# Kernel tuning notes

Measured on AMD Instinct MI355X. Metric: run time of the kernel, lower is better.

## Reference

```python
import jax, jax.numpy as jnp
import numpy as np
import math

B, S, E, H, L, VOCAB, OUT = 32, 1024, 512, 8, 2, 20000, 1
D = E // H


def positional_encoding(seq_length, embed_size):
    position = jnp.arange(seq_length, dtype=jnp.float32)[:, None]
    div_term = jnp.exp(jnp.arange(0, embed_size, 2, dtype=jnp.float32) * (-math.log(10000.0) / embed_size))
    pe = jnp.zeros((seq_length, embed_size), dtype=jnp.float32)
    pe = pe.at[:, 0::2].set(jnp.sin(position * div_term))
    pe = pe.at[:, 1::2].set(jnp.cos(position * div_term))
    return pe


def setup_inputs() -> dict:
    key = jax.random.key(0)
    ks = jax.random.split(key, 12)
    inputs = jax.random.randint(ks[0], (B, S), 0, VOCAB)
    s = 1.0 / math.sqrt(E)
    embed_table = jax.random.normal(ks[1], (VOCAB, E), jnp.float32)
    embed_table = embed_table.at[0].set(0.0)  # padding_idx=0
    # per-layer Q,K,V,O linear weights [L,E,E] (applied as x @ W + b) and biases [L,E]
    Wq = jax.random.normal(ks[2], (L, E, E), jnp.float32) * s
    Wk = jax.random.normal(ks[3], (L, E, E), jnp.float32) * s
    Wv = jax.random.normal(ks[4], (L, E, E), jnp.float32) * s
    Wo = jax.random.normal(ks[5], (L, E, E), jnp.float32) * s
    bq = jax.random.normal(ks[6], (L, E), jnp.float32) * s
    bk = jax.random.normal(ks[7], (L, E), jnp.float32) * s
    bv = jax.random.normal(ks[8], (L, E), jnp.float32) * s
    bo = jax.random.normal(ks[9], (L, E), jnp.float32) * s
    W_out = jax.random.normal(ks[10], (E, OUT), jnp.float32) * s
    b_out = jax.random.normal(ks[11], (OUT,), jnp.float32) * s
    return {"inputs": inputs, "embed_table": embed_table, "Wq": Wq, "bq": bq,
            "Wk": Wk, "bk": bk, "Wv": Wv, "bv": bv, "Wo": Wo, "bo": bo,
            "W_out": W_out, "b_out": b_out}


def _mha(x, Wq, bq, Wk, bk, Wv, bv, Wo, bo, mask):
    b, s = x.shape[:2]
    def heads(W, bias):
        return (x @ W + bias).reshape(b, s, H, D).transpose(0, 2, 1, 3)  # [b,H,s,D]
    q, k, v = heads(Wq, bq), heads(Wk, bk), heads(Wv, bv)
    scores = jnp.einsum('bhqd,bhkd->bhqk', q, k) / math.sqrt(D)
    scores = jnp.where(mask, -1e9, scores)
    prob = jax.nn.softmax(scores, axis=-1)
    out = jnp.einsum('bhqk,bhkd->bhqd', prob, v)
    out = out.transpose(0, 2, 1, 3).reshape(b, s, E)
    return out @ Wo + bo


def reference(inputs, embed_table, Wq, bq, Wk, bk, Wv, bv, Wo, bo, W_out, b_out):
    embeds = embed_table[inputs]  # [B,S,E]
    embeds = embeds + positional_encoding(inputs.shape[1], embeds.shape[-1])
    mask = jnp.triu(jnp.ones((inputs.shape[1], inputs.shape[1]), bool), k=1)  # future mask
    out = embeds
    for l in range(L):
        attn = _mha(out, Wq[l], bq[l], Wk[l], bk[l], Wv[l], bv[l], Wo[l], bo[l], mask)
        out = out + jax.nn.relu(attn)  # dropout is identity (eval / p=0)
    return out @ W_out + b_out
```

## Files before the change

kernel.cpp:

```cpp
#include <hip/hip_runtime.h>

typedef unsigned short u16;
typedef unsigned int u32;
using short8  = __attribute__((ext_vector_type(8))) short;
using floatx4 = __attribute__((ext_vector_type(4))) float;

#define NB 32
#define SEQ 1024
#define EMB 512
#define NH 8
#define HD 64
#define NLAYER 2
#define M_ROWS (NB * SEQ)

__device__ __forceinline__ float bf2f(u16 u) {
  union { u32 i; float f; } v; v.i = ((u32)u) << 16; return v.f;
}
__device__ __forceinline__ u16 f2bf(float f) {
  union { float f; u32 i; } v; v.f = f;
  u32 r = v.i + 0x7fffu + ((v.i >> 16) & 1u);
  return (u16)(r >> 16);
}

#if __has_builtin(__builtin_amdgcn_exp2f)
#define EXP2F __builtin_amdgcn_exp2f
#else
#define EXP2F exp2f
#endif

typedef __attribute__((address_space(3))) unsigned int lds_u32_t;
typedef __attribute__((address_space(1))) const unsigned int gbl_u32_t;
__device__ __forceinline__ void gload16(void* lds, const void* g) {
  gbl_u32_t* gp = (gbl_u32_t*)(unsigned long long)g;
  lds_u32_t* lp = (lds_u32_t*)(unsigned int)(unsigned long long)lds;
  __builtin_amdgcn_global_load_lds(gp, lp, 16, 0, 0);
}

__global__ void prep_weights(const float* __restrict__ Wq, const float* __restrict__ Wk,
                             const float* __restrict__ Wv, const float* __restrict__ Wo,
                             u16* __restrict__ WtQKV, u16* __restrict__ WtO) {
  int idx = blockIdx.x * 256 + threadIdx.x;
  const int QKV_TOT = NLAYER * 3 * EMB * EMB;
  if (idx < QKV_TOT) {
    int l = idx / (3 * EMB * EMB);
    int rem = idx % (3 * EMB * EMB);
    int n = rem / EMB, kk = rem % EMB;
    int w = n >> 9, e = n & 511;
    const float* src = (w == 0) ? Wq : (w == 1) ? Wk : Wv;
    WtQKV[idx] = f2bf(src[((size_t)l * EMB + kk) * EMB + e]);
  } else {
    int j = idx - QKV_TOT;
    int l = j / (EMB * EMB);
    int rem = j % (EMB * EMB);
    int n = rem / EMB, kk = rem % EMB;
    WtO[j] = f2bf(Wo[((size_t)l * EMB + kk) * EMB + n]);
  }
}

__global__ void embed_pe(const int* __restrict__ inp, const float* __restrict__ table,
                         u16* __restrict__ x) {
  int row = blockIdx.x;
  int tok = inp[row];
  int s = row & (SEQ - 1);
  const float negln = -9.210340371976184f / (float)EMB;
  for (int e = threadIdx.x; e < EMB; e += blockDim.x) {
    float val = table[(size_t)tok * EMB + e];
    int i = e >> 1;
    float dt = __expf((float)(2 * i) * negln);
    float ang = (float)s * dt;
    float pe = (e & 1) ? __cosf(ang) : __sinf(ang);
    x[(size_t)row * EMB + e] = f2bf(val + pe);
  }
}

#define BK 32

__global__ __launch_bounds__(256) void gemm_bt(
    const u16* __restrict__ A, const u16* __restrict__ Bt, int K, int mode,
    const float* bias0, const float* bias1, const float* bias2,
    u16* out0, u16* out1, u16* out2, const u16* resid, int Nstride) {
  __shared__ u16 sA[2][128][BK];
  __shared__ u16 sB[2][128][BK];
  int tid = threadIdx.x;
  int wave = tid >> 6, lane = tid & 63;
  int quad = lane >> 4, l16 = lane & 15;
  int wm = wave >> 1, wn = wave & 1;

  int NT = (mode == 0) ? 12 : 4;
  int blk = blockIdx.x;
  int xcd = blk & 7, slot = blk >> 3;
  int mtl = slot / NT, ntl = slot % NT;
  int bm0 = (xcd * 32 + mtl) * 128;
  int bn0 = ntl * 128;
  bool vswap = (mode == 0) && (bn0 >= 1024);

  floatx4 acc[4][4];
#pragma unroll
  for (int i = 0; i < 4; ++i)
#pragma unroll
    for (int j = 0; j < 4; ++j) acc[i][j] = (floatx4){0.f, 0.f, 0.f, 0.f};

  int rb = wave * 32;
  int lrow = lane >> 2;
  int gcg = ((lane & 3) ^ ((lane >> 3) & 3)) * 8;
  int rsl = (quad ^ ((l16 >> 1) & 3)) * 8;

  const u16* Arow0 = &A[(size_t)(bm0 + rb + lrow) * K + gcg];
  const u16* Arow1 = &A[(size_t)(bm0 + rb + 16 + lrow) * K + gcg];
  const u16* Brow0 = &Bt[(size_t)(bn0 + rb + lrow) * K + gcg];
  const u16* Brow1 = &Bt[(size_t)(bn0 + rb + 16 + lrow) * K + gcg];

  gload16(&sA[0][rb][0],      Arow0);
  gload16(&sA[0][rb + 16][0], Arow1);
  gload16(&sB[0][rb][0],      Brow0);
  gload16(&sB[0][rb + 16][0], Brow1);

  const int niter = K / BK;
  int ibuf = 0;
  for (int it = 0; it < niter; ++it) {
    if (it + 1 < niter) {
      int k1 = (it + 1) * BK;
      int nb = ibuf ^ 1;
      gload16(&sA[nb][rb][0],      Arow0 + k1);
      gload16(&sA[nb][rb + 16][0], Arow1 + k1);
      gload16(&sB[nb][rb][0],      Brow0 + k1);
      gload16(&sB[nb][rb + 16][0], Brow1 + k1);
      asm volatile("s_waitcnt vmcnt(4)" ::: "memory");
    } else {
      asm volatile("s_waitcnt vmcnt(0)" ::: "memory");
    }
    asm volatile("s_barrier" ::: "memory");

    short8 af[4], bfr[4];
#pragma unroll
    for (int mi = 0; mi < 4; ++mi)
      af[mi] = *(const short8*)&sA[ibuf][wm * 64 + mi * 16 + l16][rsl];
#pragma unroll
    for (int ni = 0; ni < 4; ++ni)
      bfr[ni] = *(const short8*)&sB[ibuf][wn * 64 + ni * 16 + l16][rsl];
    if (!vswap) {
#pragma unroll
      for (int mi = 0; mi < 4; ++mi)
#pragma unroll
        for (int ni = 0; ni < 4; ++ni)
          acc[mi][ni] = __builtin_amdgcn_mfma_f32_16x16x32_bf16(af[mi], bfr[ni], acc[mi][ni], 0, 0, 0);
    } else {
#pragma unroll
      for (int mi = 0; mi < 4; ++mi)
#pragma unroll
        for (int ni = 0; ni < 4; ++ni)
          acc[mi][ni] = __builtin_amdgcn_mfma_f32_16x16x32_bf16(bfr[ni], af[mi], acc[mi][ni], 0, 0, 0);
    }
    asm volatile("s_waitcnt lgkmcnt(0)" ::: "memory");
    asm volatile("s_barrier" ::: "memory");
    ibuf ^= 1;
  }

  u16* scr = ((u16*)sA) + wave * (16 * 68);
  int erow = lane >> 5;
  int dcol = lane & 31;

  if (!vswap) {
    int w = bn0 >> 9;
    const float* bp = (mode == 1) ? bias0 : ((w == 0) ? bias0 : bias1);
    float sc = (mode == 0 && w == 0) ? 0.18033688011112042f : 1.0f;
    float bv[4];
#pragma unroll
    for (int ni = 0; ni < 4; ++ni)
      bv[ni] = bp[(bn0 + wn * 64 + ni * 16 + l16) & 511];

#pragma unroll
    for (int mi = 0; mi < 4; ++mi) {
#pragma unroll
      for (int ni = 0; ni < 4; ++ni)
#pragma unroll
        for (int r = 0; r < 4; ++r) {
          float t = (acc[mi][ni][r] + bv[ni]) * sc;
          if (mode == 1) t = fmaxf(t, 0.f);
          scr[(quad * 4 + r) * 68 + ni * 16 + l16] = f2bf(t);
        }
      asm volatile("s_waitcnt lgkmcnt(0)" ::: "memory");

      int m0 = bm0 + wm * 64 + mi * 16;
      int colg = bn0 + wn * 64 + dcol * 2;
#pragma unroll
      for (int p = 0; p < 8; ++p) {
        int row = p * 2 + erow;
        u32 d2 = *(const u32*)&scr[row * 68 + dcol * 2];
        int m = m0 + row;
        if (mode == 0) {
          int e = colg & 511, h = e >> 6, d = e & 63;
          int b = m >> 10, sid = m & 1023;
          u16* optr = (w == 0) ? out0 : out1;
          *(u32*)&optr[((size_t)(b * NH + h) * SEQ + sid) * HD + d] = d2;
        } else {
          size_t off = (size_t)m * Nstride + colg;
          u32 rs = *(const u32*)&resid[off];
          float lo = bf2f((u16)d2) + bf2f((u16)rs);
          float hi = bf2f((u16)(d2 >> 16)) + bf2f((u16)(rs >> 16));
          *(u32*)&out0[off] = ((u32)f2bf(hi) << 16) | f2bf(lo);
        }
      }
      asm volatile("s_waitcnt lgkmcnt(0)" ::: "memory");
    }
  } else {
    float bvv[4][4];
#pragma unroll
    for (int ni = 0; ni < 4; ++ni)
#pragma unroll
      for (int r = 0; r < 4; ++r)
        bvv[ni][r] = bias2[(bn0 + wn * 64 + ni * 16 + quad * 4 + r) & 511];

    int b = (bm0 + wm * 64) >> 10;
    int sid0 = (bm0 + wm * 64) & 1023;
    int n0 = bn0 + wn * 64;
    int h = (n0 >> 6) & 7;
#pragma unroll
    for (int ni = 0; ni < 4; ++ni) {
#pragma unroll
      for (int mi = 0; mi < 4; ++mi)
#pragma unroll
        for (int r = 0; r < 4; ++r)
          scr[(quad * 4 + r) * 68 + mi * 16 + l16] = f2bf(acc[mi][ni][r] + bvv[ni][r]);
      asm volatile("s_waitcnt lgkmcnt(0)" ::: "memory");

      int d0 = (n0 & 63) + ni * 16;
#pragma unroll
      for (int p = 0; p < 8; ++p) {
        int row = p * 2 + erow;
        u32 d2 = *(const u32*)&scr[row * 68 + dcol * 2];
        *(u32*)&out2[((size_t)(b * NH + h) * HD + d0 + row) * SEQ + sid0 + dcol * 2] = d2;
      }
      asm volatile("s_waitcnt lgkmcnt(0)" ::: "memory");
    }
  }
}

#define RD8(T, row, cg) (*(const short8*)&(T)[(size_t)(row) * 64 + ((((cg) ^ ((row) & 7))) * 8)])

__global__ __launch_bounds__(256) void attn_kernel(
    const u16* __restrict__ q, const u16* __restrict__ k, const u16* __restrict__ vt,
    u16* __restrict__ o) {
  int blk = blockIdx.x;
  int xcd = blk & 7, slot = blk >> 3;
  int bh = xcd * 32 + (slot >> 3);
  int qtp = 7 - (slot & 7);
  int b = bh >> 3, h = bh & 7;
  int qA0 = qtp * 128, qB0 = qA0 + 64;

  __shared__ u16 smem[25088];
  u16* sQ = smem;
  u16* sK = smem;
  u16* sV = smem + 8192;
  u16* sP = smem + 16384;

  int tid = threadIdx.x, wave = tid >> 6, lane = tid & 63;
  int quad = lane >> 4, l16 = lane & 15;
  int rr = lane >> 3, gc8 = ((lane & 7) ^ rr) * 8;

  const u16* qbase = &q[((size_t)bh * SEQ + qA0) * HD];
  const u16* kbase = &k[(size_t)bh * SEQ * HD];
  const u16* vbase = &vt[(size_t)bh * HD * SEQ];

#pragma unroll
  for (int c = 0; c < 2; ++c) {
    int row0 = wave * 16 + c * 8;
    gload16(sQ + row0 * 64,        qbase + (size_t)(row0 + rr) * HD + gc8);
    gload16(sQ + (64 + row0) * 64, qbase + (size_t)(64 + row0 + rr) * HD + gc8);
  }
  asm volatile("s_waitcnt vmcnt(0)" ::: "memory");
  asm volatile("s_barrier" ::: "memory");
  short8 aqA0, aqA1, aqB0, aqB1;
  {
    int ra = wave * 16 + l16;
    aqA0 = RD8(sQ, ra, quad);
    aqA1 = RD8(sQ, ra, 4 + quad);
    aqB0 = RD8(sQ + 4096, ra, quad);
    aqB1 = RD8(sQ + 4096, ra, 4 + quad);
  }
  asm volatile("s_waitcnt lgkmcnt(0)" ::: "memory");
  asm volatile("s_barrier" ::: "memory");

  const u16* kp0 = kbase + (size_t)(wave * 16 + rr) * HD + gc8;
  const u16* kp1 = kp0 + 8 * HD;
  const u16* vp0 = vbase + (size_t)(wave * 16 + rr) * SEQ + gc8;
  const u16* vp1 = vp0 + 8 * SEQ;

  short8 ones;
#pragma unroll
  for (int j = 0; j < 8; ++j) ones[j] = (short)0x3F80;

  floatx4 accoA[4], accoB[4], accsumA, accsumB;
#pragma unroll
  for (int i = 0; i < 4; ++i) {
    accoA[i] = (floatx4){0.f, 0.f, 0.f, 0.f};
    accoB[i] = (floatx4){0.f, 0.f, 0.f, 0.f};
  }
  accsumA = (floatx4){0.f, 0.f, 0.f, 0.f};
  accsumB = (floatx4){0.f, 0.f, 0.f, 0.f};

  auto process = [&](short8 aq0, short8 aq1, int qX0, bool diag, int sub,
                     floatx4* acco, floatx4& accsum, int k0,
                     const u16* Kc, const u16* Vc) {
    floatx4 accs[4];
#pragma unroll
    for (int i = 0; i < 4; ++i) accs[i] = (floatx4){0.f, 0.f, 0.f, 0.f};
#pragma unroll
    for (int nt = 0; nt < 4; ++nt) {
      int rbk = nt * 16 + l16;
      accs[nt] = __builtin_amdgcn_mfma_f32_16x16x32_bf16(aq0, RD8(Kc, rbk, quad), accs[nt], 0, 0, 0);
      accs[nt] = __builtin_amdgcn_mfma_f32_16x16x32_bf16(aq1, RD8(Kc, rbk, 4 + quad), accs[nt], 0, 0, 0);
    }
    int prowbase = sub * 4352 + (wave * 16 + quad * 4) * 68;
    if (!diag) {
#pragma unroll
      for (int nt = 0; nt < 4; ++nt)
#pragma unroll
        for (int r = 0; r < 4; ++r) {
          float p = EXP2F(fminf(accs[nt][r], 108.f));
          sP[prowbase + r * 68 + nt * 16 + l16] = (u16)(__float_as_uint(p) >> 16);
        }
    } else {
      int qg_base = qX0 + wave * 16 + quad * 4;
#pragma unroll
      for (int nt = 0; nt < 4; ++nt) {
        int kg = k0 + nt * 16 + l16;
#pragma unroll
        for (int r = 0; r < 4; ++r) {
          float p = EXP2F(fminf(accs[nt][r], 108.f));
          if (kg > qg_base + r) p = 0.f;
          sP[prowbase + r * 68 + nt * 16 + l16] = (u16)(__float_as_uint(p) >> 16);
        }
      }
    }
    asm volatile("s_waitcnt lgkmcnt(0)" ::: "memory");
#pragma unroll
    for (int cst = 0; cst < 2; ++cst) {
      short8 ap = *(const short8*)&sP[sub * 4352 + (wave * 16 + l16) * 68 + cst * 32 + quad * 8];
#pragma unroll
      for (int dt = 0; dt < 4; ++dt) {
        int rv = dt * 16 + l16;
        acco[dt] = __builtin_amdgcn_mfma_f32_16x16x32_bf16(ap, RD8(Vc, rv, cst * 4 + quad), acco[dt], 0, 0, 0);
      }
      accsum = __builtin_amdgcn_mfma_f32_16x16x32_bf16(ap, ones, accsum, 0, 0, 0);
    }
  };

  {
    int row0 = wave * 16;
    gload16(sK + row0 * 64,       kp0);
    gload16(sK + (row0 + 8) * 64, kp1);
    gload16(sV + row0 * 64,       vp0);
    gload16(sV + (row0 + 8) * 64, vp1);
  }

  int ktmax = 2 * qtp + 1;
  int cur = 0;
  for (int kt = 0; kt <= ktmax; ++kt) {
    if (kt < ktmax) {
      int nb = cur ^ 1;
      size_t ko = (size_t)(kt + 1) * (64 * HD);
      size_t vo = (size_t)(kt + 1) * 64;
      int row0 = wave * 16;
      gload16(sK + nb * 4096 + row0 * 64,       kp0 + ko);
      gload16(sK + nb * 4096 + (row0 + 8) * 64, kp1 + ko);
      gload16(sV + nb * 4096 + row0 * 64,       vp0 + vo);
      gload16(sV + nb * 4096 + (row0 + 8) * 64, vp1 + vo);
      asm volatile("s_waitcnt vmcnt(4)" ::: "memory");
    } else {
      asm volatile("s_waitcnt vmcnt(0)" ::: "memory");
    }
    asm volatile("s_barrier" ::: "memory");

    const u16* Kc = sK + cur * 4096;
    const u16* Vc = sV + cur * 4096;
    int k0 = kt * 64;
    if (kt <= 2 * qtp)
      process(aqA0, aqA1, qA0, kt == 2 * qtp, 0, accoA, accsumA, k0, Kc, Vc);
    process(aqB0, aqB1, qB0, kt == ktmax, 1, accoB, accsumB, k0, Kc, Vc);

    asm volatile("s_waitcnt lgkmcnt(0)" ::: "memory");
    asm volatile("s_barrier" ::: "memory");
    cur ^= 1;
  }

#pragma unroll
  for (int dt = 0; dt < 4; ++dt)
#pragma unroll
    for (int r = 0; r < 4; ++r) {
      int rowoff = wave * 16 + quad * 4 + r;
      int col = h * HD + dt * 16 + l16;
      o[((size_t)b * SEQ + qA0 + rowoff) * EMB + col] = f2bf(accoA[dt][r] / accsumA[r]);
      o[((size_t)b * SEQ + qB0 + rowoff) * EMB + col] = f2bf(accoB[dt][r] / accsumB[r]);
    }
}

__global__ __launch_bounds__(256) void out_proj(const u16* __restrict__ x,
                                                const float* __restrict__ wout,
                                                const float* __restrict__ bout,
                                                float* __restrict__ out) {
  int wave = threadIdx.x >> 6, lane = threadIdx.x & 63;
  int m = blockIdx.x * 4 + wave;
  union { uint4 vv; u16 s[8]; } xv;
  xv.vv = *(const uint4*)&x[(size_t)m * EMB + lane * 8];
  float4 w0 = *(const float4*)&wout[lane * 8];
  float4 w1 = *(const float4*)&wout[lane * 8 + 4];
  float wv[8] = {w0.x, w0.y, w0.z, w0.w, w1.x, w1.y, w1.z, w1.w};
  float s = 0.f;
#pragma unroll
  for (int j = 0; j < 8; ++j) s += bf2f(xv.s[j]) * wv[j];
#pragma unroll
  for (int sh = 1; sh < 64; sh <<= 1) s += __shfl_xor(s, sh, 64);
  if (lane == 0) out[m] = s + bout[0];
}

extern "C" void kernel_launch(void* const* d_in, const int* in_sizes, int n_in,
                              void* d_out, int out_size, void* d_ws, size_t ws_size,
                              hipStream_t stream) {
  const int*   inp   = (const int*)d_in[0];
  const float* table = (const float*)d_in[1];
  const float* Wq    = (const float*)d_in[2];
  const float* bq    = (const float*)d_in[3];
  const float* Wk    = (const float*)d_in[4];
  const float* bk    = (const float*)d_in[5];
  const float* Wv    = (const float*)d_in[6];
  const float* bv    = (const float*)d_in[7];
  const float* Wo    = (const float*)d_in[8];
  const float* bo    = (const float*)d_in[9];
  const float* Wout  = (const float*)d_in[10];
  const float* bout  = (const float*)d_in[11];
  float* outp = (float*)d_out;

  char* ws = (char*)d_ws;
  const size_t SZ = (size_t)M_ROWS * EMB * 2;
  u16* x      = (u16*)(ws);
  u16* qb     = (u16*)(ws + SZ);
  u16* kb     = (u16*)(ws + 2 * SZ);
  u16* vb     = (u16*)(ws + 3 * SZ);
  u16* attn_b = (u16*)(ws + 4 * SZ);
  u16* WtQKV  = (u16*)(ws + 5 * SZ);
  u16* WtO    = (u16*)(ws + 5 * SZ + (size_t)NLAYER * 3 * EMB * EMB * 2);

  prep_weights<<<8192, 256, 0, stream>>>(Wq, Wk, Wv, Wo, WtQKV, WtO);
  embed_pe<<<M_ROWS, 256, 0, stream>>>(inp, table, x);

  for (int l = 0; l < NLAYER; ++l) {
    gemm_bt<<<3072, 256, 0, stream>>>(
        x, WtQKV + (size_t)l * 3 * EMB * EMB, EMB, 0,
        bq + l * EMB, bk + l * EMB, bv + l * EMB, qb, kb, vb, nullptr, 0);
    attn_kernel<<<2048, 256, 0, stream>>>(qb, kb, vb, attn_b);
    gemm_bt<<<1024, 256, 0, stream>>>(
        attn_b, WtO + (size_t)l * EMB * EMB, EMB, 1,
        bo + l * EMB, nullptr, nullptr, x, nullptr, nullptr, x, EMB);
  }
  out_proj<<<8192, 256, 0, stream>>>(x, Wout, bout, outp);
}
```

Measured before the change: 688.7 us.

## Drop K/V double buffering and share P buffer to halve attention LDS

```diff
diff --git a/kernel.cpp b/kernel.cpp
--- a/kernel.cpp
+++ b/kernel.cpp
@@ -248,11 +248,11 @@
   int b = bh >> 3, h = bh & 7;
   int qA0 = qtp * 128, qB0 = qA0 + 64;
 
-  __shared__ u16 smem[25088];
+  __shared__ u16 smem[12544];
   u16* sQ = smem;
   u16* sK = smem;
-  u16* sV = smem + 8192;
-  u16* sP = smem + 16384;
+  u16* sV = smem + 4096;
+  u16* sP = smem + 8192;
 
   int tid = threadIdx.x, wave = tid >> 6, lane = tid & 63;
   int quad = lane >> 4, l16 = lane & 15;
@@ -268,8 +268,7 @@
     gload16(sQ + row0 * 64,        qbase + (size_t)(row0 + rr) * HD + gc8);
     gload16(sQ + (64 + row0) * 64, qbase + (size_t)(64 + row0 + rr) * HD + gc8);
   }
-  asm volatile("s_waitcnt vmcnt(0)" ::: "memory");
-  asm volatile("s_barrier" ::: "memory");
+  __syncthreads();
   short8 aqA0, aqA1, aqB0, aqB1;
   {
     int ra = wave * 16 + l16;
@@ -278,8 +277,7 @@
     aqB0 = RD8(sQ + 4096, ra, quad);
     aqB1 = RD8(sQ + 4096, ra, 4 + quad);
   }
-  asm volatile("s_waitcnt lgkmcnt(0)" ::: "memory");
-  asm volatile("s_barrier" ::: "memory");
+  __syncthreads();
 
   const u16* kp0 = kbase + (size_t)(wave * 16 + rr) * HD + gc8;
   const u16* kp1 = kp0 + 8 * HD;
@@ -299,19 +297,19 @@
   accsumA = (floatx4){0.f, 0.f, 0.f, 0.f};
   accsumB = (floatx4){0.f, 0.f, 0.f, 0.f};
 
-  auto process = [&](short8 aq0, short8 aq1, int qX0, bool diag, int sub,
-                     floatx4* acco, floatx4& accsum, int k0,
-                     const u16* Kc, const u16* Vc) {
+  auto process = [&](short8 aq0, short8 aq1, int qX0, bool diag,
+                     floatx4* acco, floatx4& accsum, int k0) {
     floatx4 accs[4];
 #pragma unroll
     for (int i = 0; i < 4; ++i) accs[i] = (floatx4){0.f, 0.f, 0.f, 0.f};
 #pragma unroll
     for (int nt = 0; nt < 4; ++nt) {
       int rbk = nt * 16 + l16;
-      accs[nt] = __builtin_amdgcn_mfma_f32_16x16x32_bf16(aq0, RD8(Kc, rbk, quad), accs[nt], 0, 0, 0);
-      accs[nt] = __builtin_amdgcn_mfma_f32_16x16x32_bf16(aq1, RD8(Kc, rbk, 4 + quad), accs[nt], 0, 0, 0);
-    }
-    int prowbase = sub * 4352 + (wave * 16 + quad * 4) * 68;
+      accs[nt] = __builtin_amdgcn_mfma_f32_16x16x32_bf16(aq0, RD8(sK, rbk, quad), accs[nt], 0, 0, 0);
+      accs[nt] = __builtin_amdgcn_mfma_f32_16x16x32_bf16(aq1, RD8(sK, rbk, 4 + quad), accs[nt], 0, 0, 0);
+    }
+    asm volatile("s_waitcnt lgkmcnt(0)" ::: "memory");
+    int prowbase = (wave * 16 + quad * 4) * 68;
     if (!diag) {
 #pragma unroll
       for (int nt = 0; nt < 4; ++nt)
@@ -336,52 +334,35 @@
     asm volatile("s_waitcnt lgkmcnt(0)" ::: "memory");
 #pragma unroll
     for (int cst = 0; cst < 2; ++cst) {
-      short8 ap = *(const short8*)&sP[sub * 4352 + (wave * 16 + l16) * 68 + cst * 32 + quad * 8];
+      short8 ap = *(const short8*)&sP[(wave * 16 + l16) * 68 + cst * 32 + quad * 8];
 #pragma unroll
       for (int dt = 0; dt < 4; ++dt) {
         int rv = dt * 16 + l16;
-        acco[dt] = __builtin_amdgcn_mfma_f32_16x16x32_bf16(ap, RD8(Vc, rv, cst * 4 + quad), acco[dt], 0, 0, 0);
+        acco[dt] = __builtin_amdgcn_mfma_f32_16x16x32_bf16(ap, RD8(sV, rv, cst * 4 + quad), acco[dt], 0, 0, 0);
       }
       accsum = __builtin_amdgcn_mfma_f32_16x16x32_bf16(ap, ones, accsum, 0, 0, 0);
     }
   };
 
-  {
-    int row0 = wave * 16;
-    gload16(sK + row0 * 64,       kp0);
-    gload16(sK + (row0 + 8) * 64, kp1);
-    gload16(sV + row0 * 64,       vp0);
-    gload16(sV + (row0 + 8) * 64, vp1);
-  }
-
   int ktmax = 2 * qtp + 1;
-  int cur = 0;
   for (int kt = 0; kt <= ktmax; ++kt) {
-    if (kt < ktmax) {
-      int nb = cur ^ 1;
-      size_t ko = (size_t)(kt + 1) * (64 * HD);
-      size_t vo = (size_t)(kt + 1) * 64;
+    {
+      size_t ko = (size_t)kt * (64 * HD);
+      size_t vo = (size_t)kt * 64;
       int row0 = wave * 16;
-      gload16(sK + nb * 4096 + row0 * 64,       kp0 + ko);
-      gload16(sK + nb * 4096 + (row0 + 8) * 64, kp1 + ko);
-      gload16(sV + nb * 4096 + row0 * 64,       vp0 + vo);
-      gload16(sV + nb * 4096 + (row0 + 8) * 64, vp1 + vo);
-      asm volatile("s_waitcnt vmcnt(4)" ::: "memory");
-    } else {
-      asm volatile("s_waitcnt vmcnt(0)" ::: "memory");
-    }
-    asm volatile("s_barrier" ::: "memory");
-
-    const u16* Kc = sK + cur * 4096;
-    const u16* Vc = sV + cur * 4096;
+      gload16(sK + row0 * 64,       kp0 + ko);
+      gload16(sK + (row0 + 8) * 64, kp1 + ko);
+      gload16(sV + row0 * 64,       vp0 + vo);
+      gload16(sV + (row0 + 8) * 64, vp1 + vo);
+    }
+    __syncthreads();
+
     int k0 = kt * 64;
     if (kt <= 2 * qtp)
-      process(aqA0, aqA1, qA0, kt == 2 * qtp, 0, accoA, accsumA, k0, Kc, Vc);
-    process(aqB0, aqB1, qB0, kt == ktmax, 1, accoB, accsumB, k0, Kc, Vc);
-
-    asm volatile("s_waitcnt lgkmcnt(0)" ::: "memory");
-    asm volatile("s_barrier" ::: "memory");
-    cur ^= 1;
+      process(aqA0, aqA1, qA0, kt == 2 * qtp, accoA, accsumA, k0);
+    process(aqB0, aqB1, qB0, kt == ktmax, accoB, accsumB, k0);
+
+    __syncthreads();
   }
 
 #pragma unroll
```

Measured after the change: 677.6 us. About the same (-1.6%).
